# Optimization experiments

Measured on AMD Instinct MI355X. Metric: run time of the kernel, lower is better.

## Reference

```python
import jax, jax.numpy as jnp
import numpy as np

B, L, D, H, E = 64, 128, 768, 2, 131072  # graphs, nodes/graph, hidden, heads, edges
N = B * L
C = D // H  # per-head channels


def _transformer_conv(x, src, dst, wq, bq, wk, bk, wv, bv, ws, bs):
    # PyG TransformerConv (concat=True, root_weight=True, beta=False)
    n = x.shape[0]
    q = (x @ wq + bq).reshape(n, H, C)
    k = (x @ wk + bk).reshape(n, H, C)
    v = (x @ wv + bv).reshape(n, H, C)
    # per-edge attention logits [E, H]
    logits = jnp.sum(q[dst] * k[src], axis=-1) * (1.0 / np.sqrt(C))
    # scatter softmax over incoming edges of each dst node
    m = jax.ops.segment_max(logits, dst, num_segments=n)
    e = jnp.exp(logits - m[dst])
    s = jax.ops.segment_sum(e, dst, num_segments=n)
    alpha = e / s[dst]  # [E, H]
    msg = alpha[..., None] * v[src]  # [E, H, C]
    agg = jax.ops.segment_sum(msg, dst, num_segments=n).reshape(n, D)
    return agg + x @ ws + bs


def setup_inputs() -> dict:
    key = jax.random.key(0)
    ks = jax.random.split(key, 24)
    x = jax.random.normal(ks[0], (N, D), jnp.float32)
    # within-graph random edges
    dst = jax.random.randint(ks[1], (E,), 0, N)
    off = jax.random.randint(ks[2], (E,), 0, L)
    src = (dst // L) * L + off
    edge_index = jnp.stack([src, dst]).astype(jnp.int32)

    def lin(k, i, o):
        return jax.random.normal(k, (i, o), jnp.float32) * 0.02

    inp = {"x": x, "edge_index": edge_index}
    i = 3
    for layer in ("1", "2"):
        for nm in ("wq", "wk", "wv", "ws"):
            inp[nm + layer] = lin(ks[i], D, D); i += 1
            inp["b" + nm[1] + layer] = jnp.zeros((D,), jnp.float32)
    inp["atti_w"] = lin(ks[i], 2 * D, D); i += 1
    inp["atti_b"] = jnp.zeros((D,), jnp.float32)
    inp["atts_w"] = lin(ks[i], D, 1); i += 1
    inp["atts_b"] = jnp.zeros((1,), jnp.float32)
    inp["fc1_w"] = lin(ks[i], D, D); i += 1
    inp["fc1_b"] = jnp.zeros((D,), jnp.float32)
    inp["fc2_w"] = lin(ks[i], D, 3); i += 1
    inp["fc2_b"] = jnp.zeros((3,), jnp.float32)
    return inp


def reference(x, edge_index, wq1, bq1, wk1, bk1, wv1, bv1, ws1, bs1,
              wq2, bq2, wk2, bk2, wv2, bv2, ws2, bs2,
              atti_w, atti_b, atts_w, atts_b, fc1_w, fc1_b, fc2_w, fc2_b):
    src, dst = edge_index[0], edge_index[1]
    h = jax.nn.relu(_transformer_conv(x, src, dst, wq1, bq1, wk1, bk1, wv1, bv1, ws1, bs1))
    h = jax.nn.relu(_transformer_conv(h, src, dst, wq2, bq2, wk2, bk2, wv2, bv2, ws2, bs2))
    # pad(): equal-size graphs -> reshape, mask all-valid (x_mask all False)
    hp = h.reshape(B, L, D)
    # attention pooling (eval path): query = first node of each graph
    x_q = jnp.broadcast_to(hp[:, :1], hp.shape)  # [B, L, D]
    x_c = jax.nn.relu(jnp.concatenate([x_q, hp], axis=-1) @ atti_w + atti_b)
    score = x_c @ atts_w + atts_b  # [B, L, 1]
    score = jax.nn.softmax(score, axis=1)
    pooled = jnp.sum(hp * score, axis=1)  # [B, D]
    out = jnp.tanh(pooled @ fc1_w + fc1_b) @ fc2_w + fc2_b
    return jax.nn.log_softmax(out, axis=-1)
```

## Files before the change

### kernel.cpp

```cpp
#include <hip/hip_runtime.h>

#define NN 8192
#define DD 768
#define EE 131072
#define BBg 64
#define LLn 128
#define CCh 384

typedef unsigned short u16;
typedef unsigned char u8;
typedef __attribute__((ext_vector_type(8))) short short8;
typedef __attribute__((ext_vector_type(4))) float f32x4;

__device__ __forceinline__ float b2f(u16 u) {
    union { unsigned int i; float f; } x; x.i = ((unsigned int)u) << 16; return x.f;
}
__device__ __forceinline__ u16 f2b(float f) {
    union { float f; unsigned int i; } x; x.f = f;
    unsigned int r = x.i + 0x7fffu + ((x.i >> 16) & 1u);
    return (u16)(r >> 16);
}
__device__ __forceinline__ void gload16(const void* g, void* l) {
    __builtin_amdgcn_global_load_lds((const __attribute__((address_space(1))) void*)g,
                                     (__attribute__((address_space(3))) void*)l, 16, 0, 0);
}

__global__ void cnt_build(const int* __restrict__ srcp, const int* __restrict__ dstp,
                          unsigned int* __restrict__ cnt32) {
    int e = blockIdx.x * 256 + threadIdx.x;
    int d = dstp[e], s = srcp[e];
    int g = d >> 7;
    int idx = (g << 14) + ((d & 127) << 7) + (s & 127);
    atomicAdd(&cnt32[idx >> 2], 1u << ((idx & 3) * 8));
}

__global__ void f32_to_bf16_vec(const float* __restrict__ in, u16* __restrict__ out, int n4) {
    int i = blockIdx.x * 256 + threadIdx.x;
    if (i >= n4) return;
    float4 v = ((const float4*)in)[i];
    ushort4 o; o.x = f2b(v.x); o.y = f2b(v.y); o.z = f2b(v.z); o.w = f2b(v.w);
    ((ushort4*)out)[i] = o;
}

struct TP { const float* src; u16* dst; int rowOff; };
struct TP11 { TP a[11]; };

__global__ __launch_bounds__(256) void transpose_batched(TP11 args) {
    __shared__ float tile[64][65];
    TP tp = args.a[blockIdx.z];
    int n0 = blockIdx.x * 64, k0 = blockIdx.y * 64;
    int t = threadIdx.x;
    int tc = t & 63, tr = t >> 6;
#pragma unroll
    for (int i = 0; i < 16; i++)
        tile[tr + i * 4][tc] = tp.src[(size_t)(tp.rowOff + k0 + tr + i * 4) * DD + n0 + tc];
    __syncthreads();
#pragma unroll
    for (int i = 0; i < 16; i++) {
        int row = tr + i * 4;
        tp.dst[(size_t)(n0 + row) * DD + k0 + tc] = f2b(tile[tc][row]);
    }
}

enum { EPI_F32 = 1, EPI_TANH = 3 };

__global__ __launch_bounds__(256) void gemm_bf16(const u16* __restrict__ A,
                                                 const u16* __restrict__ Wt,
                                                 const float* __restrict__ bias,
                                                 void* __restrict__ outp, int K, int mode) {
    __shared__ u16 As[64][72];
    __shared__ u16 Bs[64][72];
    const int m0 = blockIdx.y * 64, n0 = blockIdx.x * 64;
    const int t = threadIdx.x;
    const int lane = t & 63, w = t >> 6;
    const int tr = t >> 2, tc = (t & 3) * 16;
    f32x4 acc[4] = {{0,0,0,0},{0,0,0,0},{0,0,0,0},{0,0,0,0}};
    const int fRow = lane & 15;
    const int fK = (lane >> 4) * 8;

    for (int k0 = 0; k0 < K; k0 += 64) {
        int4 a0 = *(const int4*)(A + (size_t)(m0 + tr) * K + k0 + tc);
        int4 a1 = *(const int4*)(A + (size_t)(m0 + tr) * K + k0 + tc + 8);
        int4 b0 = *(const int4*)(Wt + (size_t)(n0 + tr) * K + k0 + tc);
        int4 b1 = *(const int4*)(Wt + (size_t)(n0 + tr) * K + k0 + tc + 8);
        __syncthreads();
        *(int4*)&As[tr][tc] = a0; *(int4*)&As[tr][tc + 8] = a1;
        *(int4*)&Bs[tr][tc] = b0; *(int4*)&Bs[tr][tc + 8] = b1;
        __syncthreads();
#pragma unroll
        for (int s = 0; s < 2; s++) {
            short8 af = *(const short8*)&As[w * 16 + fRow][s * 32 + fK];
#pragma unroll
            for (int g = 0; g < 4; g++) {
                short8 bf = *(const short8*)&Bs[g * 16 + fRow][s * 32 + fK];
                acc[g] = __builtin_amdgcn_mfma_f32_16x16x32_bf16(af, bf, acc[g], 0, 0, 0);
            }
        }
    }
    const int colLocal = lane & 15;
    const int rowLocal = (lane >> 4) * 4;
#pragma unroll
    for (int g = 0; g < 4; g++) {
        int col = n0 + g * 16 + colLocal;
        float bv = bias ? bias[col] : 0.f;
#pragma unroll
        for (int i = 0; i < 4; i++) {
            int row = m0 + w * 16 + rowLocal + i;
            float v = acc[g][i] + bv;
            if (mode == EPI_TANH) v = tanhf(v);
            ((float*)outp)[(size_t)row * DD + col] = v;
        }
    }
}

__global__ __launch_bounds__(256, 2) void gemm256(const u16* __restrict__ A,
                                                  const u16* __restrict__ Wt,
                                                  const float* __restrict__ b0,
                                                  const float* __restrict__ b1,
                                                  const float* __restrict__ b2,
                                                  const float* __restrict__ b3,
                                                  u16* __restrict__ o0, u16* __restrict__ o1,
                                                  u16* __restrict__ o2, u16* __restrict__ o3) {
    __shared__ u16 As[256 * 64];
    __shared__ u16 Bs[128 * 64];
    const int K = DD;
    const int t = threadIdx.x;
    const int lane = t & 63, w = t >> 6;
    const int wr = w >> 1, wc = w & 1;
    const int m0 = blockIdx.y * 256, n0 = blockIdx.x * 128;
    const int fRow = lane & 15, fThr = lane >> 4;
    f32x4 acc[8][4] = {};
    const u16* Abase = A + (size_t)m0 * K;
    const u16* Bbase = Wt + (size_t)n0 * K;

    for (int k0 = 0; k0 < K; k0 += 64) {
        __syncthreads();
#pragma unroll
        for (int i = 0; i < 8; i++) {
            int c = t + 256 * i;
            int row = c >> 3;
            int col = ((c & 7) ^ (row & 7)) * 8;
            gload16(Abase + (size_t)row * K + k0 + col, (char*)As + (size_t)c * 16);
        }
#pragma unroll
        for (int i = 0; i < 4; i++) {
            int c = t + 256 * i;
            int row = c >> 3;
            int col = ((c & 7) ^ (row & 7)) * 8;
            gload16(Bbase + (size_t)row * K + k0 + col, (char*)Bs + (size_t)c * 16);
        }
        __syncthreads();
#pragma unroll
        for (int kk = 0; kk < 64; kk += 32) {
            const int cjW = (kk >> 3) + fThr;
            short8 af[8], bf[4];
#pragma unroll
            for (int i = 0; i < 8; i++) {
                int R = wr * 128 + i * 16 + fRow;
                af[i] = *(const short8*)&As[(R * 8 + (cjW ^ (R & 7))) * 8];
            }
#pragma unroll
            for (int g = 0; g < 4; g++) {
                int R = wc * 64 + g * 16 + fRow;
                bf[g] = *(const short8*)&Bs[(R * 8 + (cjW ^ (R & 7))) * 8];
            }
#pragma unroll
            for (int i = 0; i < 8; i++)
#pragma unroll
                for (int g = 0; g < 4; g++)
                    acc[i][g] = __builtin_amdgcn_mfma_f32_16x16x32_bf16(af[i], bf[g], acc[i][g], 0, 0, 0);
        }
    }
    const int chunk = (n0 + wc * 64) / DD;
    const float* bp = (chunk == 0) ? b0 : (chunk == 1) ? b1 : (chunk == 2) ? b2 : b3;
    u16* op = (chunk == 0) ? o0 : (chunk == 1) ? o1 : (chunk == 2) ? o2 : o3;
    const int cb = n0 + wc * 64 - chunk * DD;
    if (chunk == 2) {
#pragma unroll
        for (int g = 0; g < 4; g++) {
            int col = cb + g * 16 + fRow;
            float bv = bp[col];
#pragma unroll
            for (int i = 0; i < 8; i++) {
                int rowb = m0 + wr * 128 + i * 16 + fThr * 4;
                ushort4 st;
                st.x = f2b(acc[i][g][0] + bv);
                st.y = f2b(acc[i][g][1] + bv);
                st.z = f2b(acc[i][g][2] + bv);
                st.w = f2b(acc[i][g][3] + bv);
                *(ushort4*)(op + (size_t)col * NN + rowb) = st;
            }
        }
    } else {
#pragma unroll
        for (int g = 0; g < 4; g++) {
            int col = cb + g * 16 + fRow;
            float bv = bp[col];
#pragma unroll
            for (int i = 0; i < 8; i++) {
                int rowb = m0 + wr * 128 + i * 16 + fThr * 4;
#pragma unroll
                for (int rr = 0; rr < 4; rr++)
                    op[(size_t)(rowb + rr) * DD + col] = f2b(acc[i][g][rr] + bv);
            }
        }
    }
}

__global__ __launch_bounds__(256) void gemm_xc(const u16* __restrict__ A,
                                               const u16* __restrict__ Wt,
                                               const u16* __restrict__ wt8,
                                               const float* __restrict__ atti_b,
                                               const float* __restrict__ atts_w,
                                               float* __restrict__ score) {
    __shared__ u16 As[128 * 64];
    __shared__ u16 Bs[128 * 64];
    __shared__ float aq_p[2][128];
    const int K = DD;
    const int t = threadIdx.x;
    const int lane = t & 63, w = t >> 6;
    const int wr = w >> 1, wc = w & 1;
    const int n0 = blockIdx.x * 128, m0 = blockIdx.y * 128;
    const int fRow = lane & 15, fThr = lane >> 4;

    {
        int col = t & 127, kh = t >> 7;
        const u16* xr = A + (size_t)m0 * DD + kh * 384;
        const u16* wr8 = wt8 + (size_t)(n0 + col) * DD + kh * 384;
        float s = 0.f;
#pragma unroll 8
        for (int j = 0; j < 96; j++) {
            ushort4 a4 = *(const ushort4*)(xr + j * 4);
            ushort4 b4 = *(const ushort4*)(wr8 + j * 4);
            s += b2f(a4.x) * b2f(b4.x) + b2f(a4.y) * b2f(b4.y)
               + b2f(a4.z) * b2f(b4.z) + b2f(a4.w) * b2f(b4.w);
        }
        aq_p[kh][col] = s;
    }

    f32x4 acc[4][4] = {};
    const u16* Abase = A + (size_t)m0 * K;
    const u16* Bbase = Wt + (size_t)n0 * K;
    for (int k0 = 0; k0 < K; k0 += 64) {
        __syncthreads();
#pragma unroll
        for (int i = 0; i < 4; i++) {
            int c = t + 256 * i;
            int row = c >> 3;
            int col = ((c & 7) ^ (row & 7)) * 8;
            gload16(Abase + (size_t)row * K + k0 + col, (char*)As + (size_t)c * 16);
            gload16(Bbase + (size_t)row * K + k0 + col, (char*)Bs + (size_t)c * 16);
        }
        __syncthreads();
#pragma unroll
        for (int kk = 0; kk < 64; kk += 32) {
            const int cjW = (kk >> 3) + fThr;
            short8 af[4], bf[4];
#pragma unroll
            for (int i = 0; i < 4; i++) {
                int R = wr * 64 + i * 16 + fRow;
                af[i] = *(const short8*)&As[(R * 8 + (cjW ^ (R & 7))) * 8];
            }
#pragma unroll
            for (int g = 0; g < 4; g++) {
                int R = wc * 64 + g * 16 + fRow;
                bf[g] = *(const short8*)&Bs[(R * 8 + (cjW ^ (R & 7))) * 8];
            }
#pragma unroll
            for (int i = 0; i < 4; i++)
#pragma unroll
                for (int g = 0; g < 4; g++)
                    acc[i][g] = __builtin_amdgcn_mfma_f32_16x16x32_bf16(af[i], bf[g], acc[i][g], 0, 0, 0);
        }
    }
    float rsum[4][4] = {};
#pragma unroll
    for (int g = 0; g < 4; g++) {
        int cl = wc * 64 + g * 16 + fRow;
        int col = n0 + cl;
        float bv = atti_b[col] + aq_p[0][cl] + aq_p[1][cl];
        float av = atts_w[col];
#pragma unroll
        for (int i = 0; i < 4; i++)
#pragma unroll
            for (int rr = 0; rr < 4; rr++) {
                float v = fmaxf(acc[i][g][rr] + bv, 0.f);
                rsum[i][rr] += v * av;
            }
    }
#pragma unroll
    for (int i = 0; i < 4; i++)
#pragma unroll
        for (int rr = 0; rr < 4; rr++) {
            float s = rsum[i][rr];
            s += __shfl_xor(s, 1, 16); s += __shfl_xor(s, 2, 16);
            s += __shfl_xor(s, 4, 16); s += __shfl_xor(s, 8, 16);
            if (fRow == 0)
                atomicAdd(&score[m0 + wr * 64 + i * 16 + fThr * 4 + rr], s);
        }
}

__global__ __launch_bounds__(256) void attn_qk(const u16* __restrict__ qb,
                                               const u16* __restrict__ kb,
                                               const u8* __restrict__ cnt,
                                               u16* __restrict__ P) {
    __shared__ u16 As[64][72];
    __shared__ u16 Bs[128][72];
    __shared__ u16 Pl[64][136];
    const int half = blockIdx.x, hd = blockIdx.y, g = blockIdx.z;
    const int t = threadIdx.x;
    const int lane = t & 63, w = t >> 6;
    const int fRow = lane & 15, fThr = lane >> 4;
    const int dstBase = g * 128 + half * 64;
    const u16* Qb = qb + (size_t)dstBase * DD + hd * CCh;
    const u16* Kb = kb + (size_t)(g * 128) * DD + hd * CCh;

    f32x4 acc[8] = {};
    const int trA = t >> 2, tcA = (t & 3) * 16;
    const int trB = t >> 1, tcB = (t & 1) * 32;
    for (int k0 = 0; k0 < CCh; k0 += 64) {
        int4 a0 = *(const int4*)(Qb + (size_t)trA * DD + k0 + tcA);
        int4 a1 = *(const int4*)(Qb + (size_t)trA * DD + k0 + tcA + 8);
        int4 b0 = *(const int4*)(Kb + (size_t)trB * DD + k0 + tcB);
        int4 b1 = *(const int4*)(Kb + (size_t)trB * DD + k0 + tcB + 8);
        int4 b2 = *(const int4*)(Kb + (size_t)trB * DD + k0 + tcB + 16);
        int4 b3 = *(const int4*)(Kb + (size_t)trB * DD + k0 + tcB + 24);
        __syncthreads();
        *(int4*)&As[trA][tcA] = a0; *(int4*)&As[trA][tcA + 8] = a1;
        *(int4*)&Bs[trB][tcB] = b0; *(int4*)&Bs[trB][tcB + 8] = b1;
        *(int4*)&Bs[trB][tcB + 16] = b2; *(int4*)&Bs[trB][tcB + 24] = b3;
        __syncthreads();
#pragma unroll
        for (int kk = 0; kk < 64; kk += 32) {
            short8 af = *(const short8*)&As[w * 16 + fRow][kk + fThr * 8];
#pragma unroll
            for (int j = 0; j < 8; j++) {
                short8 bf = *(const short8*)&Bs[j * 16 + fRow][kk + fThr * 8];
                acc[j] = __builtin_amdgcn_mfma_f32_16x16x32_bf16(af, bf, acc[j], 0, 0, 0);
            }
        }
    }

    const float scale = 0.05103103630798288f;
    const u8* cg = cnt + ((size_t)g << 14);
    const int rbase = half * 64 + w * 16 + fThr * 4;
    float pv[8][4];
#pragma unroll
    for (int i = 0; i < 4; i++) {
        float m = -3.4e38f;
#pragma unroll
        for (int j = 0; j < 8; j++) {
            float c = (float)cg[(rbase + i) * 128 + j * 16 + fRow];
            float s = acc[j][i] * scale;
            pv[j][i] = c;
            if (c > 0.f) m = fmaxf(m, s);
        }
#pragma unroll
        for (int msk = 1; msk <= 8; msk <<= 1) m = fmaxf(m, __shfl_xor(m, msk, 16));
        float sum = 0.f;
#pragma unroll
        for (int j = 0; j < 8; j++) {
            float p = (pv[j][i] > 0.f) ? pv[j][i] * __expf(acc[j][i] * scale - m) : 0.f;
            pv[j][i] = p; sum += p;
        }
#pragma unroll
        for (int msk = 1; msk <= 8; msk <<= 1) sum += __shfl_xor(sum, msk, 16);
        float inv = (sum > 0.f) ? 1.f / sum : 0.f;
#pragma unroll
        for (int j = 0; j < 8; j++)
            Pl[w * 16 + fThr * 4 + i][j * 16 + fRow] = f2b(pv[j][i] * inv);
    }
    __syncthreads();
    u16* Pbase = P + ((size_t)(g * 2 + hd) * 128 + half * 64) * 128;
#pragma unroll
    for (int ii = 0; ii < 4; ii++) {
        int c = t + 256 * ii;
        int row = c >> 4, ch = c & 15;
        *(short8*)(Pbase + (size_t)row * 128 + ch * 8) = *(const short8*)&Pl[row][ch * 8];
    }
}

__global__ __launch_bounds__(256) void attn_pv(const u16* __restrict__ P,
                                               const u16* __restrict__ vT,
                                               const u16* __restrict__ hs,
                                               u16* __restrict__ out) {
    __shared__ u16 Vt[64][136];
    const int cc = blockIdx.x, hd = blockIdx.y, g = blockIdx.z;
    const int t = threadIdx.x;
    const int lane = t & 63, w = t >> 6;
    const int fRow = lane & 15, fThr = lane >> 4;
    const u16* Pbase = P + (size_t)(g * 2 + hd) * 128 * 128;

#pragma unroll
    for (int ii = 0; ii < 4; ii++) {
        int q = t + 256 * ii;
        int row = q >> 4, col = (q & 15) * 8;
        *(int4*)&Vt[row][col] =
            *(const int4*)(vT + (size_t)(hd * CCh + cc * 64 + row) * NN + g * 128 + col);
    }
    __syncthreads();

    f32x4 acc[2][4] = {};
#pragma unroll
    for (int kk = 0; kk < 128; kk += 32) {
        short8 af[2], bf[4];
#pragma unroll
        for (int i = 0; i < 2; i++) {
            int row = w * 32 + i * 16 + fRow;
            af[i] = *(const short8*)(Pbase + (size_t)row * 128 + kk + fThr * 8);
        }
#pragma unroll
        for (int j = 0; j < 4; j++)
            bf[j] = *(const short8*)&Vt[j * 16 + fRow][kk + fThr * 8];
#pragma unroll
        for (int i = 0; i < 2; i++)
#pragma unroll
            for (int j = 0; j < 4; j++)
                acc[i][j] = __builtin_amdgcn_mfma_f32_16x16x32_bf16(af[i], bf[j], acc[i][j], 0, 0, 0);
    }
#pragma unroll
    for (int j = 0; j < 4; j++) {
        int col = hd * CCh + cc * 64 + j * 16 + fRow;
#pragma unroll
        for (int i = 0; i < 2; i++) {
            int rowb = w * 32 + i * 16 + fThr * 4;
#pragma unroll
            for (int rr = 0; rr < 4; rr++) {
                int row = g * 128 + rowb + rr;
                size_t idx = (size_t)row * DD + col;
                float r = fmaxf(acc[i][j][rr] + b2f(hs[idx]), 0.f);
                out[idx] = f2b(r);
            }
        }
    }
}

__global__ __launch_bounds__(192) void pool_kernel(const float* __restrict__ score,
                                                   const u16* __restrict__ hx,
                                                   u16* __restrict__ pb) {
    int b = blockIdx.x, t = threadIdx.x;
    __shared__ float sprob[LLn];
    if (t < 64) {
        float s0 = score[b * LLn + t];
        float s1 = score[b * LLn + 64 + t];
        float mx = fmaxf(s0, s1);
#pragma unroll
        for (int m = 1; m <= 32; m <<= 1) mx = fmaxf(mx, __shfl_xor(mx, m, 64));
        float e0 = __expf(s0 - mx), e1 = __expf(s1 - mx);
        float sum = e0 + e1;
#pragma unroll
        for (int m = 1; m <= 32; m <<= 1) sum += __shfl_xor(sum, m, 64);
        float inv = 1.f / sum;
        sprob[t] = e0 * inv; sprob[t + 64] = e1 * inv;
    }
    __syncthreads();
    int c = t * 4;
    float a0 = 0, a1 = 0, a2 = 0, a3 = 0;
    for (int l = 0; l < LLn; l++) {
        float wl = sprob[l];
        ushort4 hv = *(const ushort4*)(hx + (size_t)(b * LLn + l) * DD + c);
        a0 += wl * b2f(hv.x); a1 += wl * b2f(hv.y); a2 += wl * b2f(hv.z); a3 += wl * b2f(hv.w);
    }
    ushort4 o; o.x = f2b(a0); o.y = f2b(a1); o.z = f2b(a2); o.w = f2b(a3);
    *(ushort4*)(pb + (size_t)b * DD + c) = o;
}

__global__ __launch_bounds__(256) void head2_kernel(const float* __restrict__ u,
                                                    const float* __restrict__ fc2w,
                                                    const float* __restrict__ fc2b,
                                                    float* __restrict__ outp) {
    int b = blockIdx.x, t = threadIdx.x;
    __shared__ float sred[4][3];
    float p0 = 0, p1 = 0, p2 = 0;
    for (int k = t; k < DD; k += 256) {
        float uv = u[(size_t)b * DD + k];
        p0 += uv * fc2w[k * 3 + 0]; p1 += uv * fc2w[k * 3 + 1]; p2 += uv * fc2w[k * 3 + 2];
    }
#pragma unroll
    for (int m = 1; m <= 32; m <<= 1) {
        p0 += __shfl_xor(p0, m, 64); p1 += __shfl_xor(p1, m, 64); p2 += __shfl_xor(p2, m, 64);
    }
    int w = t >> 6, lane = t & 63;
    if (lane == 0) { sred[w][0] = p0; sred[w][1] = p1; sred[w][2] = p2; }
    __syncthreads();
    if (t == 0) {
        float z0 = fc2b[0], z1 = fc2b[1], z2 = fc2b[2];
        for (int i = 0; i < 4; i++) { z0 += sred[i][0]; z1 += sred[i][1]; z2 += sred[i][2]; }
        float mx = fmaxf(z0, fmaxf(z1, z2));
        float lse = mx + logf(__expf(z0 - mx) + __expf(z1 - mx) + __expf(z2 - mx));
        outp[b * 3 + 0] = z0 - lse; outp[b * 3 + 1] = z1 - lse; outp[b * 3 + 2] = z2 - lse;
    }
}

static inline char* carve(char*& p, size_t bytes) {
    char* r = p;
    p += (bytes + 255) & ~(size_t)255;
    return r;
}

extern "C" void kernel_launch(void* const* d_in, const int* in_sizes, int n_in,
                              void* d_out, int out_size, void* d_ws, size_t ws_size,
                              hipStream_t stream) {
    const float* x = (const float*)d_in[0];
    const int* ei = (const int*)d_in[1];
    const int* srcp = ei;
    const int* dstp = ei + EE;
    const float* wL[8] = {(const float*)d_in[2], (const float*)d_in[4], (const float*)d_in[6],
                          (const float*)d_in[8], (const float*)d_in[10], (const float*)d_in[12],
                          (const float*)d_in[14], (const float*)d_in[16]};
    const float* bL[8] = {(const float*)d_in[3], (const float*)d_in[5], (const float*)d_in[7],
                          (const float*)d_in[9], (const float*)d_in[11], (const float*)d_in[13],
                          (const float*)d_in[15], (const float*)d_in[17]};
    const float* atti_w = (const float*)d_in[18];
    const float* atti_b = (const float*)d_in[19];
    const float* atts_w = (const float*)d_in[20];
    const float* fc1_w = (const float*)d_in[22];
    const float* fc1_b = (const float*)d_in[23];
    const float* fc2_w = (const float*)d_in[24];
    const float* fc2_b = (const float*)d_in[25];
    float* outp = (float*)d_out;

    char* p = (char*)d_ws;
    const size_t ndb = (size_t)NN * DD * 2;
    const size_t wsz = (size_t)DD * DD * 2;
    u16* qb = (u16*)carve(p, ndb);
    u16* kb = (u16*)carve(p, ndb);
    u16* vt = (u16*)carve(p, ndb);
    u16* xb = (u16*)carve(p, ndb);
    u16* hb = (u16*)carve(p, ndb);
    u16* hs = (u16*)carve(p, ndb);
    u16* Pbuf = (u16*)carve(p, (size_t)BBg * 2 * 128 * 128 * 2);
    u16* wtcat1 = (u16*)carve(p, wsz * 4);
    u16* wtcat2 = (u16*)carve(p, wsz * 4);
    u16* wt8 = (u16*)carve(p, wsz);
    u16* wt9 = (u16*)carve(p, wsz);
    u16* wtfc1 = (u16*)carve(p, wsz);
    u16* pb = (u16*)carve(p, (size_t)BBg * DD * 2);
    float* uu = (float*)carve(p, (size_t)BBg * DD * 4);
    u8* cnt = (u8*)carve(p, (size_t)BBg * 128 * 128);
    float* score = (float*)carve(p, NN * 4);

    hipMemsetAsync(cnt, 0, (size_t)BBg * 128 * 128, stream);
    hipMemsetAsync(score, 0, NN * 4, stream);
    cnt_build<<<EE / 256, 256, 0, stream>>>(srcp, dstp, (unsigned int*)cnt);

    f32_to_bf16_vec<<<(NN * DD / 4) / 256, 256, 0, stream>>>(x, xb, NN * DD / 4);
    TP11 tps;
    for (int i = 0; i < 4; i++) tps.a[i] = {wL[i], wtcat1 + (size_t)i * DD * DD, 0};
    for (int i = 0; i < 4; i++) tps.a[4 + i] = {wL[4 + i], wtcat2 + (size_t)i * DD * DD, 0};
    tps.a[8] = {atti_w, wt8, 0};
    tps.a[9] = {atti_w, wt9, DD};
    tps.a[10] = {fc1_w, wtfc1, 0};
    transpose_batched<<<dim3(12, 12, 11), 256, 0, stream>>>(tps);

    dim3 gf(24, 32);
    dim3 gq(2, 2, BBg);
    dim3 gp(6, 2, BBg);
    gemm256<<<gf, 256, 0, stream>>>(xb, wtcat1, bL[0], bL[1], bL[2], bL[3], qb, kb, vt, hs);
    attn_qk<<<gq, 256, 0, stream>>>(qb, kb, cnt, Pbuf);
    attn_pv<<<gp, 256, 0, stream>>>(Pbuf, vt, hs, hb);
    gemm256<<<gf, 256, 0, stream>>>(hb, wtcat2, bL[4], bL[5], bL[6], bL[7], qb, kb, vt, hs);
    attn_qk<<<gq, 256, 0, stream>>>(qb, kb, cnt, Pbuf);
    attn_pv<<<gp, 256, 0, stream>>>(Pbuf, vt, hs, xb);

    gemm_xc<<<dim3(6, 64), 256, 0, stream>>>(xb, wt9, wt8, atti_b, atts_w, score);
    pool_kernel<<<BBg, 192, 0, stream>>>(score, xb, pb);

    gemm_bf16<<<dim3(12, 1), 256, 0, stream>>>(pb, wtfc1, fc1_b, uu, DD, EPI_TANH);
    head2_kernel<<<BBg, 256, 0, stream>>>(uu, fc2_w, fc2_b, outp);
}
```

Measured before the change: 367.2 us.

## Split fused QK-softmax into tiled logits kernel and separate softmax kernel

The fused attn_qk kernel, which computed 64x128 logit tiles and did a masked softmax in registers, is split in two. A logits kernel computes 64x64 tiles, doubling the block count to 512 per layer, and writes fp32 logits to a new global buffer. A separate softmax kernel reads those logits and the edge counts row-wise with vector loads and writes bf16 probabilities. The goal is more parallelism and fewer registers per block, at the cost of an extra kernel launch and a round trip of fp32 logits through global memory.

```diff
diff --git a/kernel.cpp b/kernel.cpp
--- a/kernel.cpp
+++ b/kernel.cpp
@@ -300,83 +300,101 @@
         }
 }
 
-__global__ __launch_bounds__(256) void attn_qk(const u16* __restrict__ qb,
-                                               const u16* __restrict__ kb,
-                                               const u8* __restrict__ cnt,
-                                               u16* __restrict__ P) {
-    __shared__ u16 As[64][72];
-    __shared__ u16 Bs[128][72];
-    __shared__ u16 Pl[64][136];
-    const int half = blockIdx.x, hd = blockIdx.y, g = blockIdx.z;
+__global__ __launch_bounds__(256) void attn_logits(const u16* __restrict__ qb,
+                                                   const u16* __restrict__ kb,
+                                                   float* __restrict__ logits) {
+    __shared__ u16 Qs[64][72];
+    __shared__ u16 Ks[64][72];
+    const int mq = blockIdx.x >> 1, nq = blockIdx.x & 1;
+    const int hd = blockIdx.y, g = blockIdx.z;
     const int t = threadIdx.x;
     const int lane = t & 63, w = t >> 6;
     const int fRow = lane & 15, fThr = lane >> 4;
-    const int dstBase = g * 128 + half * 64;
-    const u16* Qb = qb + (size_t)dstBase * DD + hd * CCh;
-    const u16* Kb = kb + (size_t)(g * 128) * DD + hd * CCh;
-
-    f32x4 acc[8] = {};
-    const int trA = t >> 2, tcA = (t & 3) * 16;
-    const int trB = t >> 1, tcB = (t & 1) * 32;
+    const u16* Qb = qb + (size_t)(g * 128 + mq * 64) * DD + hd * CCh;
+    const u16* Kb = kb + (size_t)(g * 128 + nq * 64) * DD + hd * CCh;
+    const int tr = t >> 2, tc = (t & 3) * 16;
+
+    f32x4 acc[4] = {};
     for (int k0 = 0; k0 < CCh; k0 += 64) {
-        int4 a0 = *(const int4*)(Qb + (size_t)trA * DD + k0 + tcA);
-        int4 a1 = *(const int4*)(Qb + (size_t)trA * DD + k0 + tcA + 8);
-        int4 b0 = *(const int4*)(Kb + (size_t)trB * DD + k0 + tcB);
-        int4 b1 = *(const int4*)(Kb + (size_t)trB * DD + k0 + tcB + 8);
-        int4 b2 = *(const int4*)(Kb + (size_t)trB * DD + k0 + tcB + 16);
-        int4 b3 = *(const int4*)(Kb + (size_t)trB * DD + k0 + tcB + 24);
-        __syncthreads();
-        *(int4*)&As[trA][tcA] = a0; *(int4*)&As[trA][tcA + 8] = a1;
-        *(int4*)&Bs[trB][tcB] = b0; *(int4*)&Bs[trB][tcB + 8] = b1;
-        *(int4*)&Bs[trB][tcB + 16] = b2; *(int4*)&Bs[trB][tcB + 24] = b3;
+        int4 a0 = *(const int4*)(Qb + (size_t)tr * DD + k0 + tc);
+        int4 a1 = *(const int4*)(Qb + (size_t)tr * DD + k0 + tc + 8);
+        int4 b0 = *(const int4*)(Kb + (size_t)tr * DD + k0 + tc);
+        int4 b1 = *(const int4*)(Kb + (size_t)tr * DD + k0 + tc + 8);
+        __syncthreads();
+        *(int4*)&Qs[tr][tc] = a0; *(int4*)&Qs[tr][tc + 8] = a1;
+        *(int4*)&Ks[tr][tc] = b0; *(int4*)&Ks[tr][tc + 8] = b1;
         __syncthreads();
 #pragma unroll
         for (int kk = 0; kk < 64; kk += 32) {
-            short8 af = *(const short8*)&As[w * 16 + fRow][kk + fThr * 8];
-#pragma unroll
-            for (int j = 0; j < 8; j++) {
-                short8 bf = *(const short8*)&Bs[j * 16 + fRow][kk + fThr * 8];
+            short8 af = *(const short8*)&Qs[w * 16 + fRow][kk + fThr * 8];
+#pragma unroll
+            for (int j = 0; j < 4; j++) {
+                short8 bf = *(const short8*)&Ks[j * 16 + fRow][kk + fThr * 8];
                 acc[j] = __builtin_amdgcn_mfma_f32_16x16x32_bf16(af, bf, acc[j], 0, 0, 0);
             }
         }
     }
-
     const float scale = 0.05103103630798288f;
-    const u8* cg = cnt + ((size_t)g << 14);
-    const int rbase = half * 64 + w * 16 + fThr * 4;
-    float pv[8][4];
-#pragma unroll
-    for (int i = 0; i < 4; i++) {
-        float m = -3.4e38f;
-#pragma unroll
-        for (int j = 0; j < 8; j++) {
-            float c = (float)cg[(rbase + i) * 128 + j * 16 + fRow];
-            float s = acc[j][i] * scale;
-            pv[j][i] = c;
-            if (c > 0.f) m = fmaxf(m, s);
-        }
-#pragma unroll
-        for (int msk = 1; msk <= 8; msk <<= 1) m = fmaxf(m, __shfl_xor(m, msk, 16));
-        float sum = 0.f;
-#pragma unroll
-        for (int j = 0; j < 8; j++) {
-            float p = (pv[j][i] > 0.f) ? pv[j][i] * __expf(acc[j][i] * scale - m) : 0.f;
-            pv[j][i] = p; sum += p;
-        }
-#pragma unroll
-        for (int msk = 1; msk <= 8; msk <<= 1) sum += __shfl_xor(sum, msk, 16);
-        float inv = (sum > 0.f) ? 1.f / sum : 0.f;
-#pragma unroll
-        for (int j = 0; j < 8; j++)
-            Pl[w * 16 + fThr * 4 + i][j * 16 + fRow] = f2b(pv[j][i] * inv);
-    }
-    __syncthreads();
-    u16* Pbase = P + ((size_t)(g * 2 + hd) * 128 + half * 64) * 128;
-#pragma unroll
-    for (int ii = 0; ii < 4; ii++) {
-        int c = t + 256 * ii;
-        int row = c >> 4, ch = c & 15;
-        *(short8*)(Pbase + (size_t)row * 128 + ch * 8) = *(const short8*)&Pl[row][ch * 8];
+    float* lg = logits + ((size_t)(g * 2 + hd) * 128 + mq * 64) * 128 + nq * 64;
+#pragma unroll
+    for (int j = 0; j < 4; j++) {
+        int col = j * 16 + fRow;
+#pragma unroll
+        for (int rr = 0; rr < 4; rr++) {
+            int row = w * 16 + fThr * 4 + rr;
+            lg[(size_t)row * 128 + col] = acc[j][rr] * scale;
+        }
+    }
+}
+
+__global__ __launch_bounds__(256) void attn_softmax(const float* __restrict__ logits,
+                                                    const u8* __restrict__ cnt,
+                                                    u16* __restrict__ P) {
+    const int half = blockIdx.x, hd = blockIdx.y, g = blockIdx.z;
+    const int t = threadIdx.x;
+    const int r = t >> 2, part = t & 3;
+    const int d = half * 64 + r;
+    const float* lrow = logits + ((size_t)(g * 2 + hd) * 128 + d) * 128 + part * 32;
+    const u8* crow = cnt + ((size_t)g << 14) + d * 128 + part * 32;
+
+    float lv[32];
+    unsigned int cw[8];
+    {
+        int4 c0 = *(const int4*)crow;
+        int4 c1 = *(const int4*)(crow + 16);
+        cw[0] = c0.x; cw[1] = c0.y; cw[2] = c0.z; cw[3] = c0.w;
+        cw[4] = c1.x; cw[5] = c1.y; cw[6] = c1.z; cw[7] = c1.w;
+    }
+    float m = -3.4e38f;
+#pragma unroll
+    for (int i = 0; i < 8; i++) {
+        float4 l4 = *(const float4*)(lrow + i * 4);
+        lv[i * 4 + 0] = l4.x; lv[i * 4 + 1] = l4.y; lv[i * 4 + 2] = l4.z; lv[i * 4 + 3] = l4.w;
+    }
+#pragma unroll
+    for (int i = 0; i < 32; i++) {
+        unsigned int c = (cw[i >> 2] >> ((i & 3) * 8)) & 255u;
+        if (c) m = fmaxf(m, lv[i]);
+    }
+    m = fmaxf(m, __shfl_xor(m, 1, 64));
+    m = fmaxf(m, __shfl_xor(m, 2, 64));
+    float sum = 0.f;
+#pragma unroll
+    for (int i = 0; i < 32; i++) {
+        unsigned int c = (cw[i >> 2] >> ((i & 3) * 8)) & 255u;
+        float p = c ? (float)c * __expf(lv[i] - m) : 0.f;
+        lv[i] = p; sum += p;
+    }
+    sum += __shfl_xor(sum, 1, 64);
+    sum += __shfl_xor(sum, 2, 64);
+    float inv = (sum > 0.f) ? 1.f / sum : 0.f;
+    u16* prow = P + ((size_t)(g * 2 + hd) * 128 + d) * 128 + part * 32;
+#pragma unroll
+    for (int i = 0; i < 8; i++) {
+        ushort4 st;
+        st.x = f2b(lv[i * 4 + 0] * inv); st.y = f2b(lv[i * 4 + 1] * inv);
+        st.z = f2b(lv[i * 4 + 2] * inv); st.w = f2b(lv[i * 4 + 3] * inv);
+        *(ushort4*)(prow + i * 4) = st;
     }
 }
 
@@ -530,6 +548,7 @@
     u16* hb = (u16*)carve(p, ndb);
     u16* hs = (u16*)carve(p, ndb);
     u16* Pbuf = (u16*)carve(p, (size_t)BBg * 2 * 128 * 128 * 2);
+    float* lbuf = (float*)carve(p, (size_t)BBg * 2 * 128 * 128 * 4);
     u16* wtcat1 = (u16*)carve(p, wsz * 4);
     u16* wtcat2 = (u16*)carve(p, wsz * 4);
     u16* wt8 = (u16*)carve(p, wsz);
@@ -554,13 +573,16 @@
     transpose_batched<<<dim3(12, 12, 11), 256, 0, stream>>>(tps);
 
     dim3 gf(24, 32);
-    dim3 gq(2, 2, BBg);
+    dim3 gl(4, 2, BBg);
+    dim3 gs(2, 2, BBg);
     dim3 gp(6, 2, BBg);
     gemm256<<<gf, 256, 0, stream>>>(xb, wtcat1, bL[0], bL[1], bL[2], bL[3], qb, kb, vt, hs);
-    attn_qk<<<gq, 256, 0, stream>>>(qb, kb, cnt, Pbuf);
+    attn_logits<<<gl, 256, 0, stream>>>(qb, kb, lbuf);
+    attn_softmax<<<gs, 256, 0, stream>>>(lbuf, cnt, Pbuf);
     attn_pv<<<gp, 256, 0, stream>>>(Pbuf, vt, hs, hb);
     gemm256<<<gf, 256, 0, stream>>>(hb, wtcat2, bL[4], bL[5], bL[6], bL[7], qb, kb, vt, hs);
-    attn_qk<<<gq, 256, 0, stream>>>(qb, kb, cnt, Pbuf);
+    attn_logits<<<gl, 256, 0, stream>>>(qb, kb, lbuf);
+    attn_softmax<<<gs, 256, 0, stream>>>(lbuf, cnt, Pbuf);
     attn_pv<<<gp, 256, 0, stream>>>(Pbuf, vt, hs, xb);
 
     gemm_xc<<<dim3(6, 64), 256, 0, stream>>>(xb, wt9, wt8, atti_b, atts_w, score);
```

New measurement: 377.1 us. 1.03x slower.
